# Kernel tuning notes

Measured on AMD Instinct MI355X. Metric: run time of the kernel, lower is better.

The kernel has to match this reference:

```python
import jax, jax.numpy as jnp
import numpy as np

B, NPG, H, HEADS, L, E, IN_DIM, FREQ = 4, 256, 128, 4, 6, 65536, 5, 256
N = B * NPG
C = H // HEADS  # per-head channels = 32


def _w(key, shape, fan_in):
    return jax.random.normal(key, shape, jnp.float32) * (fan_in ** -0.5)


def _ln(x):  # LayerNorm, elementwise_affine=False, eps=1e-5
    mu = jnp.mean(x, axis=-1, keepdims=True)
    var = jnp.mean((x - mu) ** 2, axis=-1, keepdims=True)
    return (x - mu) / jnp.sqrt(var + 1e-5)


def setup_inputs() -> dict:
    key = jax.random.key(0)
    ks = jax.random.split(key, 40)
    x = jax.random.normal(ks[0], (N, IN_DIM), jnp.float32)
    # edges constrained within each graph
    kg = jnp.repeat(jnp.arange(B), E // B)
    src = jax.random.randint(ks[1], (E,), 0, NPG) + kg * NPG
    dst = jax.random.randint(ks[2], (E,), 0, NPG) + kg * NPG
    edge_index = jnp.stack([src, dst]).astype(jnp.int32)
    batch = jnp.repeat(jnp.arange(B), NPG).astype(jnp.int32)
    time_matrix = jax.random.normal(ks[3], (N, N), jnp.float32)
    p = {}
    p['Wn'] = _w(ks[4], (IN_DIM, H), IN_DIM); p['bn'] = jnp.zeros((H,), jnp.float32)
    p['Wee'] = _w(ks[5], (1, 1), 1); p['bee'] = jnp.zeros((1,), jnp.float32)
    p['Wt1'] = _w(ks[6], (FREQ, H), FREQ); p['bt1'] = jnp.zeros((H,), jnp.float32)
    p['Wt2'] = _w(ks[7], (H, H), H); p['bt2'] = jnp.zeros((H,), jnp.float32)
    p['Wa'] = _w(ks[8], (L, H, 4 * H), H); p['ba'] = jnp.zeros((L, 4 * H), jnp.float32)
    p['Wq'] = _w(ks[9], (L, H, H), H); p['bq'] = jnp.zeros((L, H), jnp.float32)
    p['Wk'] = _w(ks[10], (L, H, H), H); p['bk'] = jnp.zeros((L, H), jnp.float32)
    p['Wv'] = _w(ks[11], (L, H, H), H); p['bv'] = jnp.zeros((L, H), jnp.float32)
    p['We'] = _w(ks[12], (L, 1, H), 1)  # lin_edge, bias=False in PyG
    p['Wskip'] = _w(ks[13], (L, H, H), H); p['bskip'] = jnp.zeros((L, H), jnp.float32)
    p['Wf1'] = _w(ks[14], (L, H, 2 * H), H); p['bf1'] = jnp.zeros((L, 2 * H), jnp.float32)
    p['Wf2'] = _w(ks[15], (L, 2 * H, H), 2 * H); p['bf2'] = jnp.zeros((L, H), jnp.float32)
    p['Wb'] = _w(ks[16], (H, H, H), H); p['bb'] = jnp.zeros((H,), jnp.float32)
    p['Wm1'] = _w(ks[17], (H, H), H); p['bm1'] = jnp.zeros((H,), jnp.float32)
    p['Wm2'] = _w(ks[18], (H, 4), H); p['bm2'] = jnp.zeros((4,), jnp.float32)
    return {'x': x, 'edge_index': edge_index, 'batch': batch, 't': 50,
            'time_matrix': time_matrix, **p}


def reference(x, edge_index, batch, t, time_matrix,
              Wn, bn, Wee, bee, Wt1, bt1, Wt2, bt2,
              Wa, ba, Wq, bq, Wk, bk, Wv, bv, We, Wskip, bskip,
              Wf1, bf1, Wf2, bf2, Wb, bb, Wm1, bm1, Wm2, bm2):
    h = x @ Wn + bn  # [N,H]
    # sinusoidal timestep embedding (dim=FREQ)
    half = FREQ // 2
    freqs = jnp.exp(-jnp.log(jnp.float32(10000.0)) * jnp.arange(half, dtype=jnp.float32) / half)
    targs = jnp.float32(t) * freqs
    emb = jnp.concatenate([jnp.cos(targs), jnp.sin(targs)])[None, :]  # [1,FREQ]
    t_emb = jax.nn.silu(emb @ Wt1 + bt1) @ Wt2 + bt2  # [1,H]
    t_mod = jax.nn.silu(t_emb)

    src, dst = edge_index[0], edge_index[1]
    edge_attr = time_matrix[src, dst][:, None] @ Wee + bee  # [E,1]

    inv_sqrt_c = jnp.float32(1.0 / np.sqrt(C))
    for l in range(L):
        ss = t_mod @ Wa[l] + ba[l]  # [1,4H]
        sh_msa, sc_msa, sh_mlp, sc_mlp = jnp.split(ss, 4, axis=1)
        hn = _ln(h) * (1 + sc_msa) + sh_msa
        # TransformerConv: gather per-edge Q/K/V, softmax over incoming edges of dst
        q = (hn @ Wq[l] + bq[l]).reshape(N, HEADS, C)
        k = (hn @ Wk[l] + bk[l]).reshape(N, HEADS, C)
        v = (hn @ Wv[l] + bv[l]).reshape(N, HEADS, C)
        e = (edge_attr @ We[l]).reshape(E, HEADS, C)
        kj = k[src] + e
        alpha = jnp.sum(q[dst] * kj, axis=-1) * inv_sqrt_c  # [E,HEADS]
        m = jax.ops.segment_max(alpha, dst, num_segments=N)
        a = jnp.exp(alpha - m[dst])
        s = jax.ops.segment_sum(a, dst, num_segments=N)
        a = a / (s[dst] + 1e-16)
        msg = (v[src] + e) * a[..., None]  # [E,HEADS,C]
        attn_out = jax.ops.segment_sum(msg, dst, num_segments=N).reshape(N, H)
        attn_out = attn_out + hn @ Wskip[l] + bskip[l]  # root/skip connection
        h = h + attn_out
        hn = _ln(h) * (1 + sc_mlp) + sh_mlp
        h = h + (jax.nn.gelu(hn @ Wf1[l] + bf1[l], approximate=False) @ Wf2[l] + bf2[l])

    # to_dense_batch: all graphs have NPG nodes -> reshape, full mask
    hd = h.reshape(B, NPG, H)
    # nn.Bilinear: pair[b,i,j,o] = h[b,i] @ Wb[o] @ h[b,j] + bb[o]
    tmp = jnp.einsum('bik,okl->biol', hd, Wb)  # [B,n,H,H]
    pair = jnp.einsum('biol,bjl->bijo', tmp, hd) + bb  # [B,n,n,H]
    logits = jax.nn.silu(pair @ Wm1 + bm1) @ Wm2 + bm2  # [B,n,n,4]
    return logits
```

## Files before the change

kernel.cpp:

```cpp
#include <hip/hip_runtime.h>
#include <math.h>

#define N_NODES 1024
#define HDIM 128
#define EDGES 65536
#define LAYERS 6

typedef __attribute__((ext_vector_type(8))) short bf16x8;
typedef __attribute__((ext_vector_type(4))) float f32x4;

#define OFF_H     0
#define OFF_Q     131072
#define OFF_K     262144
#define OFF_V     393216
#define OFF_SKP   524288
#define OFF_G     655360
#define OFF_SS    917504
#define OFF_EA    920576
#define OFF_CVEC  986112
#define OFF_INT   986240
#define OFF_M     1054912
#define OFF_U     3152064
#define OFF_MT    11540672
#define OFF_HB    12589248
#define OFF_WB    12654912

#define WM1T_OFF  786432

__device__ __forceinline__ float silu_f(float x) { return x / (1.f + expf(-x)); }
__device__ __forceinline__ float frcp(float x) { return __builtin_amdgcn_rcpf(x); }

__device__ __forceinline__ unsigned short f2bf(float f) {
    unsigned int u = __float_as_uint(f);
    u += 0x7FFFu + ((u >> 16) & 1u);
    return (unsigned short)(u >> 16);
}
__device__ __forceinline__ float bf2f(unsigned short s) {
    return __uint_as_float(((unsigned int)s) << 16);
}

__global__ __launch_bounds__(256) void k_ssf(const void* tptr,
    const float* __restrict__ Wt1, const float* __restrict__ bt1,
    const float* __restrict__ Wt2, const float* __restrict__ bt2,
    const float* __restrict__ bb, const float* __restrict__ Wm1, const float* __restrict__ bm1,
    const float* __restrict__ Wa, const float* __restrict__ ba,
    float* __restrict__ ss_all, float* __restrict__ cvec)
{
    __shared__ float emb_s[256];
    __shared__ float part[2][128];
    __shared__ float tmp1_s[128];
    __shared__ float tmod_s[128];
    int tid = threadIdx.x;
    int iv = *(const int*)tptr;
    float fv = __int_as_float(iv);
    float tval = (iv > -1000000 && iv < 1000000) ? (float)iv : fv;
    {
        int fi = tid & 127;
        float fr = expf(-logf(10000.f) * (float)fi / 128.f);
        float ta = tval * fr;
        emb_s[tid] = (tid < 128) ? cosf(ta) : sinf(ta);
    }
    __syncthreads();
    {
        int col = tid & 127, sl = tid >> 7;
        float p = 0.f;
#pragma unroll 8
        for (int i = sl * 128; i < sl * 128 + 128; i++) p += emb_s[i] * Wt1[i * 128 + col];
        part[sl][col] = p;
    }
    __syncthreads();
    if (tid < 128) tmp1_s[tid] = silu_f(bt1[tid] + part[0][tid] + part[1][tid]);
    __syncthreads();
    {
        int col = tid & 127, sl = tid >> 7;
        float p = 0.f;
#pragma unroll 8
        for (int i = sl * 64; i < sl * 64 + 64; i++) p += tmp1_s[i] * Wt2[i * 128 + col];
        part[sl][col] = p;
    }
    __syncthreads();
    if (tid < 128) tmod_s[tid] = silu_f(bt2[tid] + part[0][tid] + part[1][tid]);
    __syncthreads();
    {
        int idx = blockIdx.x * 256 + tid;
        int l = idx >> 9, j = idx & 511;
        float a = ba[l * 512 + j];
        const float* w = Wa + l * 65536 + j;
#pragma unroll 4
        for (int k = 0; k < 128; k++) a += tmod_s[k] * w[k * 512];
        ss_all[idx] = a;
    }
    if (blockIdx.x == 0) {
        {
            int col = tid & 127, sl = tid >> 7;
            float p = 0.f;
#pragma unroll 8
            for (int i = sl * 64; i < sl * 64 + 64; i++) p += bb[i] * Wm1[i * 128 + col];
            part[sl][col] = p;
        }
        __syncthreads();
        if (tid < 128) cvec[tid] = bm1[tid] + part[0][tid] + part[1][tid];
    }
}

__global__ __launch_bounds__(256) void k_wtrans(
    const float* __restrict__ Wq, const float* __restrict__ Wk,
    const float* __restrict__ Wv, const float* __restrict__ Wsk,
    const float* __restrict__ Wf1, const float* __restrict__ Wf2,
    const float* __restrict__ Wm1, short* __restrict__ WT)
{
    __shared__ __align__(16) short T[64][80];
    int t = blockIdx.x;
    int tid = threadIdx.x;
    const float* src; short* dst; int K, N, kt, nt;
    if (t < 96) {
        int mat = t >> 2, sub = t & 3;
        int l = mat >> 2, m = mat & 3;
        src = (m == 0 ? Wq : m == 1 ? Wk : m == 2 ? Wv : Wsk) + l * 16384;
        dst = WT + (size_t)mat * 16384;
        K = 128; N = 128; kt = sub >> 1; nt = sub & 1;
    } else if (t < 144) {
        int i = t - 96; int l = i >> 3, sub = i & 7;
        src = Wf1 + l * 32768;
        dst = WT + 24 * 16384 + (size_t)l * 32768;
        K = 128; N = 256; kt = sub & 1; nt = sub >> 1;
    } else if (t < 192) {
        int i = t - 144; int l = i >> 3, sub = i & 7;
        src = Wf2 + l * 32768;
        dst = WT + 24 * 16384 + 6 * 32768 + (size_t)l * 32768;
        K = 256; N = 128; kt = sub >> 1; nt = sub & 1;
    } else {
        int sub = t - 192;
        src = Wm1;
        dst = WT + WM1T_OFF;
        K = 128; N = 128; kt = sub >> 1; nt = sub & 1;
    }
    int k0 = kt * 64, n0 = nt * 64;
    for (int p = 0; p < 16; p++) {
        int idx = p * 256 + tid;
        int kk = idx >> 6, nn = idx & 63;
        T[nn][kk] = (short)f2bf(src[(k0 + kk) * N + n0 + nn]);
    }
    __syncthreads();
    for (int p = 0; p < 2; p++) {
        int idx = p * 256 + tid;
        int nn = idx >> 3, sq = idx & 7;
        *(int4*)&dst[(size_t)(n0 + nn) * K + k0 + sq * 8] = *(const int4*)&T[nn][sq * 8];
    }
}

__global__ __launch_bounds__(256) void k_inpedge(const float* __restrict__ x,
    const float* __restrict__ Wn, const float* __restrict__ bn, float* __restrict__ h,
    const int* __restrict__ ei, const float* __restrict__ tm,
    const float* __restrict__ Wee, const float* __restrict__ bee,
    float* __restrict__ ea, int* __restrict__ deg)
{
    int bid = blockIdx.x;
    int tid = threadIdx.x;
    if (bid < 512) {
        int idx = bid * 256 + tid;
        int i = idx >> 7, j = idx & 127;
        float acc = bn[j];
#pragma unroll
        for (int kk = 0; kk < 5; kk++) acc += x[i * 5 + kk] * Wn[kk * 128 + j];
        h[idx] = acc;
    } else {
        int e = (bid - 512) * 256 + tid;
        int s = ei[e], d = ei[EDGES + e];
        ea[e] = tm[s * N_NODES + d] * Wee[0] + bee[0];
        atomicAdd(&deg[d], 1);
    }
}

__global__ __launch_bounds__(1024) void k_scan(const int* __restrict__ deg, int* __restrict__ rowptr)
{
    __shared__ int tmp[1024];
    int tid = threadIdx.x;
    tmp[tid] = deg[tid];
    __syncthreads();
    for (int off = 1; off < 1024; off <<= 1) {
        int vv = (tid >= off) ? tmp[tid - off] : 0;
        __syncthreads();
        tmp[tid] += vv;
        __syncthreads();
    }
    rowptr[tid + 1] = tmp[tid];
    if (tid == 0) rowptr[0] = 0;
}

__global__ __launch_bounds__(256) void k_scatter(const int* __restrict__ ei,
    const int* __restrict__ rowptr, int* __restrict__ cursor, int* __restrict__ eorder)
{
    int e = blockIdx.x * 256 + threadIdx.x;
    int d = ei[EDGES + e];
    int pos = atomicAdd(&cursor[d], 1);
    eorder[rowptr[d] + pos] = e;
}

__global__ __launch_bounds__(128) void k_sort2(const int* __restrict__ rowptr,
    int* __restrict__ eorder, const int* __restrict__ ei, const float* __restrict__ ea,
    int* __restrict__ src_csr, float* __restrict__ ea_csr)
{
    __shared__ int key[256];
    int node = blockIdx.x;
    int tid = threadIdx.x;
    int beg = rowptr[node], end = rowptr[node + 1];
    int n = end - beg;
    if (n <= 256) {
        for (int i = tid; i < 256; i += 128) key[i] = (i < n) ? eorder[beg + i] : 0x7FFFFFFF;
        __syncthreads();
        for (int k = 2; k <= 256; k <<= 1) {
            for (int j = k >> 1; j > 0; j >>= 1) {
                int i = ((tid / j) * 2 * j) + (tid % j);
                int l = i + j;
                bool up = ((i & k) == 0);
                int a = key[i], b = key[l];
                if ((a > b) == up) { key[i] = b; key[l] = a; }
                __syncthreads();
            }
        }
        for (int i = tid; i < n; i += 128) {
            int e = key[i];
            src_csr[beg + i] = ei[e];
            ea_csr[beg + i] = ea[e];
        }
    } else {
        if (tid == 0) {
            for (int i = beg + 1; i < end; ++i) {
                int kk = eorder[i];
                int j = i - 1;
                while (j >= beg && eorder[j] > kk) { eorder[j + 1] = eorder[j]; --j; }
                eorder[j + 1] = kk;
            }
        }
        __syncthreads();
        for (int i = tid; i < n; i += 128) {
            int e = eorder[beg + i];
            src_csr[beg + i] = ei[e];
            ea_csr[beg + i] = ea[e];
        }
    }
}

__global__ __launch_bounds__(256) void k_qkvs(const float* __restrict__ h,
    const float* __restrict__ ss, const short* __restrict__ WT, int layer,
    const float* __restrict__ bq, const float* __restrict__ bk,
    const float* __restrict__ bv, const float* __restrict__ bsk,
    float* __restrict__ q, short* __restrict__ kb16, short* __restrict__ vb16,
    float* __restrict__ skp)
{
    __shared__ __align__(16) short As[16][136];
    __shared__ float shs[128], scs[128];
    int tid = threadIdx.x;
    int r0 = blockIdx.x * 16;
    if (tid < 128) { shs[tid] = ss[tid]; scs[tid] = ss[128 + tid]; }
    __syncthreads();
    {
        int row = tid >> 4, o = tid & 15;
        const float* hr = h + (size_t)(r0 + row) * 128 + o * 8;
        float s = 0.f, s2 = 0.f;
#pragma unroll
        for (int j = 0; j < 2; j++) {
            float4 vv = *(const float4*)&hr[j * 4];
            s += vv.x + vv.y + vv.z + vv.w;
            s2 += vv.x * vv.x + vv.y * vv.y + vv.z * vv.z + vv.w * vv.w;
        }
        s += __shfl_xor(s, 1, 64); s2 += __shfl_xor(s2, 1, 64);
        s += __shfl_xor(s, 2, 64); s2 += __shfl_xor(s2, 2, 64);
        s += __shfl_xor(s, 4, 64); s2 += __shfl_xor(s2, 4, 64);
        s += __shfl_xor(s, 8, 64); s2 += __shfl_xor(s2, 8, 64);
        float mu = s * (1.f / 128.f);
        float var = s2 * (1.f / 128.f) - mu * mu;
        float rs = rsqrtf(var + 1e-5f);
#pragma unroll
        for (int j = 0; j < 2; j++) {
            float4 vv = *(const float4*)&hr[j * 4];
            int cb = o * 8 + j * 4;
            short4 o4;
            o4.x = (short)f2bf((vv.x - mu) * rs * (1.f + scs[cb])     + shs[cb]);
            o4.y = (short)f2bf((vv.y - mu) * rs * (1.f + scs[cb + 1]) + shs[cb + 1]);
            o4.z = (short)f2bf((vv.z - mu) * rs * (1.f + scs[cb + 2]) + shs[cb + 2]);
            o4.w = (short)f2bf((vv.w - mu) * rs * (1.f + scs[cb + 3]) + shs[cb + 3]);
            *(short4*)&As[row][cb] = o4;
        }
    }
    __syncthreads();
    int w = tid >> 6, lane = tid & 63, c = lane & 15, g = lane >> 4;
    const short* Wm = WT + (size_t)(layer * 4 + w) * 16384;
    f32x4 acc[8] = {};
#pragma unroll
    for (int kq = 0; kq < 4; kq++) {
        int ko = kq * 32 + g * 8;
        bf16x8 a0 = *(const bf16x8*)&As[c][ko];
#pragma unroll
        for (int nt = 0; nt < 8; nt++) {
            bf16x8 bfr = *(const bf16x8*)&Wm[(size_t)(nt * 16 + c) * 128 + ko];
            acc[nt] = __builtin_amdgcn_mfma_f32_16x16x32_bf16(a0, bfr, acc[nt], 0, 0, 0);
        }
    }
    if (w == 0) {
#pragma unroll
        for (int nt = 0; nt < 8; nt++) {
            int n = nt * 16 + c;
            float bv2 = bq[n];
#pragma unroll
            for (int r = 0; r < 4; r++)
                q[(size_t)(r0 + g * 4 + r) * 128 + n] = acc[nt][r] + bv2;
        }
    } else if (w == 1) {
#pragma unroll
        for (int nt = 0; nt < 8; nt++) {
            int n = nt * 16 + c;
            float bv2 = bk[n];
#pragma unroll
            for (int r = 0; r < 4; r++)
                kb16[(size_t)(r0 + g * 4 + r) * 128 + n] = (short)f2bf(acc[nt][r] + bv2);
        }
    } else if (w == 2) {
#pragma unroll
        for (int nt = 0; nt < 8; nt++) {
            int n = nt * 16 + c;
            float bv2 = bv[n];
#pragma unroll
            for (int r = 0; r < 4; r++)
                vb16[(size_t)(r0 + g * 4 + r) * 128 + n] = (short)f2bf(acc[nt][r] + bv2);
        }
    } else {
#pragma unroll
        for (int nt = 0; nt < 8; nt++) {
            int n = nt * 16 + c;
            float bv2 = bsk[n];
#pragma unroll
            for (int r = 0; r < 4; r++)
                skp[(size_t)(r0 + g * 4 + r) * 128 + n] = acc[nt][r] + bv2;
        }
    }
}

__global__ __launch_bounds__(256) void k_ffn(float* __restrict__ h,
    const short* __restrict__ WT, int layer,
    const float* __restrict__ bf1, const float* __restrict__ bf2,
    const float* __restrict__ ss2, short* __restrict__ hb, int last)
{
    __shared__ __align__(16) short As[16][136];
    __shared__ __align__(16) short Gs[16][264];
    __shared__ float shs[128], scs[128];
    int tid = threadIdx.x;
    int r0 = blockIdx.x * 16;
    if (tid < 128) { shs[tid] = ss2[tid]; scs[tid] = ss2[128 + tid]; }
    __syncthreads();
    {
        int row = tid >> 4, o = tid & 15;
        const float* hr = h + (size_t)(r0 + row) * 128 + o * 8;
        float s = 0.f, s2 = 0.f;
#pragma unroll
        for (int j = 0; j < 2; j++) {
            float4 vv = *(const float4*)&hr[j * 4];
            s += vv.x + vv.y + vv.z + vv.w;
            s2 += vv.x * vv.x + vv.y * vv.y + vv.z * vv.z + vv.w * vv.w;
        }
        s += __shfl_xor(s, 1, 64); s2 += __shfl_xor(s2, 1, 64);
        s += __shfl_xor(s, 2, 64); s2 += __shfl_xor(s2, 2, 64);
        s += __shfl_xor(s, 4, 64); s2 += __shfl_xor(s2, 4, 64);
        s += __shfl_xor(s, 8, 64); s2 += __shfl_xor(s2, 8, 64);
        float mu = s * (1.f / 128.f);
        float var = s2 * (1.f / 128.f) - mu * mu;
        float rs = rsqrtf(var + 1e-5f);
#pragma unroll
        for (int j = 0; j < 2; j++) {
            float4 vv = *(const float4*)&hr[j * 4];
            int cb = o * 8 + j * 4;
            short4 o4;
            o4.x = (short)f2bf((vv.x - mu) * rs * (1.f + scs[cb])     + shs[cb]);
            o4.y = (short)f2bf((vv.y - mu) * rs * (1.f + scs[cb + 1]) + shs[cb + 1]);
            o4.z = (short)f2bf((vv.z - mu) * rs * (1.f + scs[cb + 2]) + shs[cb + 2]);
            o4.w = (short)f2bf((vv.w - mu) * rs * (1.f + scs[cb + 3]) + shs[cb + 3]);
            *(short4*)&As[row][cb] = o4;
        }
    }
    __syncthreads();
    int w = tid >> 6, lane = tid & 63, c = lane & 15, g = lane >> 4;
    const short* W1 = WT + 24 * 16384 + (size_t)layer * 32768;
    const short* W2 = WT + 24 * 16384 + 6 * 32768 + (size_t)layer * 32768;
    {
        f32x4 acc[4] = {};
#pragma unroll
        for (int kq = 0; kq < 4; kq++) {
            int ko = kq * 32 + g * 8;
            bf16x8 a0 = *(const bf16x8*)&As[c][ko];
#pragma unroll
            for (int nt = 0; nt < 4; nt++) {
                bf16x8 bfr = *(const bf16x8*)&W1[(size_t)(w * 64 + nt * 16 + c) * 128 + ko];
                acc[nt] = __builtin_amdgcn_mfma_f32_16x16x32_bf16(a0, bfr, acc[nt], 0, 0, 0);
            }
        }
#pragma unroll
        for (int nt = 0; nt < 4; nt++) {
            int n = w * 64 + nt * 16 + c;
            float bv = bf1[n];
#pragma unroll
            for (int r = 0; r < 4; r++) {
                float y = acc[nt][r] + bv;
                float gl = 0.5f * y * (1.f + erff(y * 0.70710678118654752f));
                Gs[g * 4 + r][n] = (short)f2bf(gl);
            }
        }
    }
    __syncthreads();
    {
        f32x4 acc2[2] = {};
#pragma unroll
        for (int kq = 0; kq < 8; kq++) {
            int ko = kq * 32 + g * 8;
            bf16x8 a0 = *(const bf16x8*)&Gs[c][ko];
#pragma unroll
            for (int nt2 = 0; nt2 < 2; nt2++) {
                bf16x8 bfr = *(const bf16x8*)&W2[(size_t)(w * 32 + nt2 * 16 + c) * 256 + ko];
                acc2[nt2] = __builtin_amdgcn_mfma_f32_16x16x32_bf16(a0, bfr, acc2[nt2], 0, 0, 0);
            }
        }
#pragma unroll
        for (int nt2 = 0; nt2 < 2; nt2++) {
            int n = w * 32 + nt2 * 16 + c;
            float bv = bf2[n];
#pragma unroll
            for (int r = 0; r < 4; r++) {
                int i = r0 + g * 4 + r;
                float nv = h[(size_t)i * 128 + n] + acc2[nt2][r] + bv;
                h[(size_t)i * 128 + n] = nv;
                if (last) hb[(size_t)i * 128 + n] = (short)f2bf(nv);
            }
        }
    }
}

__global__ __launch_bounds__(256) void k_attn(const float* __restrict__ q,
    const short* __restrict__ kb16, const short* __restrict__ vb16,
    const float* __restrict__ skp, float* __restrict__ h,
    const int* __restrict__ src_csr, const float* __restrict__ ea_csr,
    const float* __restrict__ We_l, const int* __restrict__ rowptr)
{
    __shared__ float ms[3][64], ssb[3][64], a0s[3][64], a1s[3][64];
    int tid = threadIdx.x;
    int wid = tid >> 6;
    int lane = tid & 63;
    int node = blockIdx.x;
    int c0 = lane * 2;
    float2 q2 = *(const float2*)&q[node * 128 + c0];
    float we0 = We_l[c0], we1 = We_l[c0 + 1];
    int beg = rowptr[node], end = rowptr[node + 1];
    int n = end - beg;
    int tb = beg + (n * wid) / 4;
    int te = beg + (n * (wid + 1)) / 4;
    float m = -INFINITY, s = 0.f, a0 = 0.f, a1 = 0.f;
    const float isc = 0.17677669529663687f;

    int t = tb;
    for (; t + 3 < te; t += 4) {
        int sn0 = src_csr[t],     sn1 = src_csr[t + 1];
        int sn2 = src_csr[t + 2], sn3 = src_csr[t + 3];
        float e0 = ea_csr[t],     e1 = ea_csr[t + 1];
        float e2 = ea_csr[t + 2], e3 = ea_csr[t + 3];
        ushort2 ku0 = *(const ushort2*)&kb16[sn0 * 128 + c0];
        ushort2 ku1 = *(const ushort2*)&kb16[sn1 * 128 + c0];
        ushort2 ku2 = *(const ushort2*)&kb16[sn2 * 128 + c0];
        ushort2 ku3 = *(const ushort2*)&kb16[sn3 * 128 + c0];
        ushort2 vu0 = *(const ushort2*)&vb16[sn0 * 128 + c0];
        ushort2 vu1 = *(const ushort2*)&vb16[sn1 * 128 + c0];
        ushort2 vu2 = *(const ushort2*)&vb16[sn2 * 128 + c0];
        ushort2 vu3 = *(const ushort2*)&vb16[sn3 * 128 + c0];
        float p0 = q2.x * (bf2f(ku0.x) + e0 * we0) + q2.y * (bf2f(ku0.y) + e0 * we1);
        float p1 = q2.x * (bf2f(ku1.x) + e1 * we0) + q2.y * (bf2f(ku1.y) + e1 * we1);
        float p2 = q2.x * (bf2f(ku2.x) + e2 * we0) + q2.y * (bf2f(ku2.y) + e2 * we1);
        float p3 = q2.x * (bf2f(ku3.x) + e3 * we0) + q2.y * (bf2f(ku3.y) + e3 * we1);
        p0 += __shfl_xor(p0, 1, 16); p1 += __shfl_xor(p1, 1, 16);
        p2 += __shfl_xor(p2, 1, 16); p3 += __shfl_xor(p3, 1, 16);
        p0 += __shfl_xor(p0, 2, 16); p1 += __shfl_xor(p1, 2, 16);
        p2 += __shfl_xor(p2, 2, 16); p3 += __shfl_xor(p3, 2, 16);
        p0 += __shfl_xor(p0, 4, 16); p1 += __shfl_xor(p1, 4, 16);
        p2 += __shfl_xor(p2, 4, 16); p3 += __shfl_xor(p3, 4, 16);
        p0 += __shfl_xor(p0, 8, 16); p1 += __shfl_xor(p1, 8, 16);
        p2 += __shfl_xor(p2, 8, 16); p3 += __shfl_xor(p3, 8, 16);
        {
            float al = p0 * isc;
            float mn = fmaxf(m, al);
            float scale = __expf(m - mn), wq = __expf(al - mn);
            s = s * scale + wq;
            a0 = a0 * scale + wq * (bf2f(vu0.x) + e0 * we0);
            a1 = a1 * scale + wq * (bf2f(vu0.y) + e0 * we1);
            m = mn;
        }
        {
            float al = p1 * isc;
            float mn = fmaxf(m, al);
            float scale = __expf(m - mn), wq = __expf(al - mn);
            s = s * scale + wq;
            a0 = a0 * scale + wq * (bf2f(vu1.x) + e1 * we0);
            a1 = a1 * scale + wq * (bf2f(vu1.y) + e1 * we1);
            m = mn;
        }
        {
            float al = p2 * isc;
            float mn = fmaxf(m, al);
            float scale = __expf(m - mn), wq = __expf(al - mn);
            s = s * scale + wq;
            a0 = a0 * scale + wq * (bf2f(vu2.x) + e2 * we0);
            a1 = a1 * scale + wq * (bf2f(vu2.y) + e2 * we1);
            m = mn;
        }
        {
            float al = p3 * isc;
            float mn = fmaxf(m, al);
            float scale = __expf(m - mn), wq = __expf(al - mn);
            s = s * scale + wq;
            a0 = a0 * scale + wq * (bf2f(vu3.x) + e3 * we0);
            a1 = a1 * scale + wq * (bf2f(vu3.y) + e3 * we1);
            m = mn;
        }
    }
    for (; t < te; ++t) {
        int sn = src_csr[t];
        float eav = ea_csr[t];
        ushort2 ku = *(const ushort2*)&kb16[sn * 128 + c0];
        ushort2 vu = *(const ushort2*)&vb16[sn * 128 + c0];
        float part = q2.x * (bf2f(ku.x) + eav * we0) + q2.y * (bf2f(ku.y) + eav * we1);
        part += __shfl_xor(part, 1, 16);
        part += __shfl_xor(part, 2, 16);
        part += __shfl_xor(part, 4, 16);
        part += __shfl_xor(part, 8, 16);
        float alpha = part * isc;
        float mn = fmaxf(m, alpha);
        float scale = __expf(m - mn), wq = __expf(alpha - mn);
        s = s * scale + wq;
        a0 = a0 * scale + wq * (bf2f(vu.x) + eav * we0);
        a1 = a1 * scale + wq * (bf2f(vu.y) + eav * we1);
        m = mn;
    }
    if (wid > 0) {
        ms[wid - 1][lane] = m; ssb[wid - 1][lane] = s;
        a0s[wid - 1][lane] = a0; a1s[wid - 1][lane] = a1;
    }
    __syncthreads();
    if (wid == 0) {
#pragma unroll
        for (int p = 0; p < 3; p++) {
            float mB = ms[p][lane], sB = ssb[p][lane];
            float b0 = a0s[p][lane], b1 = a1s[p][lane];
            float mm = fmaxf(m, mB);
            float eA = (m  > -1e30f) ? __expf(m  - mm) : 0.f;
            float eB = (mB > -1e30f) ? __expf(mB - mm) : 0.f;
            s = s * eA + sB * eB;
            a0 = a0 * eA + b0 * eB;
            a1 = a1 * eA + b1 * eB;
            m = mm;
        }
        float inv = (s > 0.f) ? 1.f / (s + 1e-16f) : 0.f;
        int o = node * 128 + c0;
        h[o]     += skp[o]     + a0 * inv;
        h[o + 1] += skp[o + 1] + a1 * inv;
    }
}

__global__ __launch_bounds__(256) void k_mprep(const float* __restrict__ Wb,
    const short* __restrict__ WT, float* __restrict__ M)
{
    __shared__ __align__(16) short Bls[128][136];
    int tid = threadIdx.x;
    int k = blockIdx.x;
    const short* Wm1T = WT + WM1T_OFF;
    {
        int lq = (tid & 31) * 4;
        int ob = tid >> 5;
        for (int it = 0; it < 16; it++) {
            int o = it * 8 + ob;
            float4 vv = *(const float4*)&Wb[(size_t)o * 16384 + k * 128 + lq];
            Bls[lq][o]     = (short)f2bf(vv.x);
            Bls[lq + 1][o] = (short)f2bf(vv.y);
            Bls[lq + 2][o] = (short)f2bf(vv.z);
            Bls[lq + 3][o] = (short)f2bf(vv.w);
        }
    }
    __syncthreads();
    int w = tid >> 6, lane = tid & 63, c = lane & 15, g = lane >> 4;
    f32x4 acc[2][8] = {};
#pragma unroll
    for (int kq = 0; kq < 4; kq++) {
        int ko = kq * 32 + g * 8;
        bf16x8 a0 = *(const bf16x8*)&Wm1T[(size_t)(w * 32 + c) * 128 + ko];
        bf16x8 a1 = *(const bf16x8*)&Wm1T[(size_t)(w * 32 + 16 + c) * 128 + ko];
#pragma unroll
        for (int nt = 0; nt < 8; nt++) {
            bf16x8 b = *(const bf16x8*)&Bls[nt * 16 + c][ko];
            acc[0][nt] = __builtin_amdgcn_mfma_f32_16x16x32_bf16(a0, b, acc[0][nt], 0, 0, 0);
            acc[1][nt] = __builtin_amdgcn_mfma_f32_16x16x32_bf16(a1, b, acc[1][nt], 0, 0, 0);
        }
    }
    float* Mk = M + (size_t)k * 16384;
#pragma unroll
    for (int it = 0; it < 2; it++)
#pragma unroll
        for (int nt = 0; nt < 8; nt++)
#pragma unroll
            for (int r = 0; r < 4; r++) {
                int m = w * 32 + it * 16 + g * 4 + r;
                int l = nt * 16 + c;
                Mk[m * 128 + l] = acc[it][nt][r];
            }
}

__global__ __launch_bounds__(256) void k_mtrans(const float* __restrict__ M,
                                                short* __restrict__ Mt)
{
    __shared__ __align__(16) short Ts[64][136];
    int tid = threadIdx.x;
    int n0 = blockIdx.x * 64;
    for (int p = 0; p < 32; p++) {
        int idx = p * 256 + tid;
        int k = idx >> 6, nn = idx & 63;
        Ts[nn][k] = (short)f2bf(M[(size_t)k * 16384 + n0 + nn]);
    }
    __syncthreads();
    for (int p = 0; p < 4; p++) {
        int idx = p * 256 + tid;
        int nn = idx >> 4, s = idx & 15;
        *(int4*)&Mt[(size_t)(n0 + nn) * 128 + s * 8] = *(const int4*)&Ts[nn][s * 8];
    }
}

__global__ __launch_bounds__(256) void k_p1(const short* __restrict__ hb,
    const short* __restrict__ Mt, short* __restrict__ U)
{
    __shared__ __align__(16) short As[128][72];
    __shared__ __align__(16) short Bs[128][72];
    int tid = threadIdx.x;
    int n0 = blockIdx.x * 128;
    int i0 = blockIdx.y * 128;
    int w = tid >> 6, lane = tid & 63, c = lane & 15, g = lane >> 4;
    f32x4 acc[2][8] = {};
    for (int kh = 0; kh < 2; kh++) {
        __syncthreads();
        for (int idx = tid; idx < 1024; idx += 256) {
            int r = idx >> 3, s = idx & 7;
            *(int4*)&As[r][s * 8] = *(const int4*)&hb[(i0 + r) * 128 + kh * 64 + s * 8];
            *(int4*)&Bs[r][s * 8] = *(const int4*)&Mt[(size_t)(n0 + r) * 128 + kh * 64 + s * 8];
        }
        __syncthreads();
#pragma unroll
        for (int kk = 0; kk < 2; kk++) {
            int ko = kk * 32 + g * 8;
            bf16x8 a0 = *(const bf16x8*)&As[w * 32 + c][ko];
            bf16x8 a1 = *(const bf16x8*)&As[w * 32 + 16 + c][ko];
#pragma unroll
            for (int nt = 0; nt < 8; nt++) {
                bf16x8 b = *(const bf16x8*)&Bs[nt * 16 + c][ko];
                acc[0][nt] = __builtin_amdgcn_mfma_f32_16x16x32_bf16(a0, b, acc[0][nt], 0, 0, 0);
                acc[1][nt] = __builtin_amdgcn_mfma_f32_16x16x32_bf16(a1, b, acc[1][nt], 0, 0, 0);
            }
        }
    }
#pragma unroll
    for (int it = 0; it < 2; it++)
#pragma unroll
        for (int nt = 0; nt < 8; nt++)
#pragma unroll
            for (int r = 0; r < 4; r++) {
                int i = i0 + w * 32 + it * 16 + g * 4 + r;
                int n = n0 + nt * 16 + c;
                U[(size_t)i * 16384 + n] = (short)f2bf(acc[it][nt][r]);
            }
}

__global__ __launch_bounds__(256) void k_p2(const short* __restrict__ hb,
    const short* __restrict__ U, const float* __restrict__ cvec,
    const float* __restrict__ Wm2, const float* __restrict__ bm2,
    float* __restrict__ out)
{
    __shared__ __align__(16) short Us[128][136];
    __shared__ float cvs[128];
    __shared__ float w2s[128][4];
    int tid = threadIdx.x;
    int i = blockIdx.x;
    int b = i >> 8;
    int w = tid >> 6, lane = tid & 63, c = lane & 15, g = lane >> 4;
    if (tid < 128) {
        cvs[tid] = cvec[tid];
        *(float4*)&w2s[tid][0] = *(const float4*)&Wm2[tid * 4];
    }
    for (int idx = tid; idx < 2048; idx += 256) {
        int r = idx >> 4, s = idx & 15;
        *(int4*)&Us[r][s * 8] = *(const int4*)&U[(size_t)i * 16384 + r * 128 + s * 8];
    }
    __syncthreads();
    float4 bmv = *(const float4*)&bm2[0];
#pragma unroll
    for (int jt = 0; jt < 4; jt++) {
        int jbase = w * 64 + jt * 16;
        bf16x8 hf[4];
        const short* hrow = hb + (size_t)(b * 256 + jbase + c) * 128;
#pragma unroll
        for (int kq = 0; kq < 4; kq++)
            hf[kq] = *(const bf16x8*)(hrow + kq * 32 + g * 8);
        f32x4 acc[8] = {};
#pragma unroll
        for (int kq = 0; kq < 4; kq++) {
            int ko = kq * 32 + g * 8;
#pragma unroll
            for (int mt = 0; mt < 8; mt++) {
                bf16x8 uv = *(const bf16x8*)&Us[mt * 16 + c][ko];
                acc[mt] = __builtin_amdgcn_mfma_f32_16x16x32_bf16(uv, hf[kq], acc[mt], 0, 0, 0);
            }
        }
        float p0 = 0.f, p1 = 0.f, p2 = 0.f, p3 = 0.f;
#pragma unroll
        for (int mt = 0; mt < 8; mt++) {
#pragma unroll
            for (int r = 0; r < 4; r++) {
                int m = mt * 16 + g * 4 + r;
                float y = acc[mt][r] + cvs[m];
                float sv = y * frcp(1.f + __expf(-y));
                p0 += sv * w2s[m][0]; p1 += sv * w2s[m][1];
                p2 += sv * w2s[m][2]; p3 += sv * w2s[m][3];
            }
        }
        p0 += __shfl_xor(p0, 16, 64); p1 += __shfl_xor(p1, 16, 64);
        p2 += __shfl_xor(p2, 16, 64); p3 += __shfl_xor(p3, 16, 64);
        p0 += __shfl_xor(p0, 32, 64); p1 += __shfl_xor(p1, 32, 64);
        p2 += __shfl_xor(p2, 32, 64); p3 += __shfl_xor(p3, 32, 64);
        if (g == 0) {
            int j = jbase + c;
            float4 o4 = { p0 + bmv.x, p1 + bmv.y, p2 + bmv.z, p3 + bmv.w };
            *(float4*)&out[((size_t)i * 256 + j) * 4] = o4;
        }
    }
}

extern "C" void kernel_launch(void* const* d_in, const int* in_sizes, int n_in,
                              void* d_out, int out_size, void* d_ws, size_t ws_size,
                              hipStream_t stream)
{
    const float* x   = (const float*)d_in[0];
    const int*   ei  = (const int*)d_in[1];
    const void*  tptr= d_in[3];
    const float* tm  = (const float*)d_in[4];
    const float* Wn  = (const float*)d_in[5];
    const float* bn  = (const float*)d_in[6];
    const float* Wee = (const float*)d_in[7];
    const float* bee = (const float*)d_in[8];
    const float* Wt1 = (const float*)d_in[9];
    const float* bt1 = (const float*)d_in[10];
    const float* Wt2 = (const float*)d_in[11];
    const float* bt2 = (const float*)d_in[12];
    const float* Wa  = (const float*)d_in[13];
    const float* ba  = (const float*)d_in[14];
    const float* Wq  = (const float*)d_in[15];
    const float* bq  = (const float*)d_in[16];
    const float* Wk  = (const float*)d_in[17];
    const float* bk  = (const float*)d_in[18];
    const float* Wv  = (const float*)d_in[19];
    const float* bv  = (const float*)d_in[20];
    const float* We  = (const float*)d_in[21];
    const float* Wsk = (const float*)d_in[22];
    const float* bsk = (const float*)d_in[23];
    const float* Wf1 = (const float*)d_in[24];
    const float* bf1 = (const float*)d_in[25];
    const float* Wf2 = (const float*)d_in[26];
    const float* bf2 = (const float*)d_in[27];
    const float* Wb  = (const float*)d_in[28];
    const float* bb  = (const float*)d_in[29];
    const float* Wm1 = (const float*)d_in[30];
    const float* bm1 = (const float*)d_in[31];
    const float* Wm2 = (const float*)d_in[32];
    const float* bm2 = (const float*)d_in[33];
    float* out = (float*)d_out;
    float* ws = (float*)d_ws;

    float* h    = ws + OFF_H;
    float* qb   = ws + OFF_Q;
    short* kb16 = (short*)(ws + OFF_K);
    short* vb16 = (short*)(ws + OFF_V);
    float* skp  = ws + OFF_SKP;
    float* ss   = ws + OFF_SS;
    float* ea   = ws + OFF_EA;
    float* cvec = ws + OFF_CVEC;
    int* iws    = (int*)(ws + OFF_INT);
    int* deg    = iws;
    int* cursor = iws + 1024;
    int* rowptr = iws + 2048;
    int* eorder = iws + 3073;
    int* src_csr   = (int*)(ws + OFF_G);
    float* ea_csr  = ws + OFF_G + 65536;
    float* Mst  = ws + OFF_M;
    short* Ub   = (short*)(ws + OFF_U);
    short* Mtb  = (short*)(ws + OFF_MT);
    short* hbb  = (short*)(ws + OFF_HB);
    short* WT   = (short*)(ws + OFF_WB);

    hipMemsetAsync(deg, 0, 2048 * sizeof(int), stream);
    k_ssf<<<12, 256, 0, stream>>>(tptr, Wt1, bt1, Wt2, bt2, bb, Wm1, bm1, Wa, ba, ss, cvec);
    k_wtrans<<<196, 256, 0, stream>>>(Wq, Wk, Wv, Wsk, Wf1, Wf2, Wm1, WT);
    k_inpedge<<<768, 256, 0, stream>>>(x, Wn, bn, h, ei, tm, Wee, bee, ea, deg);
    k_scan<<<1, 1024, 0, stream>>>(deg, rowptr);
    k_scatter<<<256, 256, 0, stream>>>(ei, rowptr, cursor, eorder);
    k_sort2<<<1024, 128, 0, stream>>>(rowptr, eorder, ei, ea, src_csr, ea_csr);

    for (int l = 0; l < LAYERS; l++) {
        const float* ssl = ss + l * 512;
        k_qkvs<<<64, 256, 0, stream>>>(h, ssl, WT, l,
            bq + l * 128, bk + l * 128, bv + l * 128, bsk + l * 128,
            qb, kb16, vb16, skp);
        k_attn<<<1024, 256, 0, stream>>>(qb, kb16, vb16, skp, h, src_csr, ea_csr,
                                         We + l * 128, rowptr);
        k_ffn<<<64, 256, 0, stream>>>(h, WT, l, bf1 + l * 256, bf2 + l * 128,
                                      ssl + 256, hbb, l == LAYERS - 1);
    }

    k_mprep<<<128, 256, 0, stream>>>(Wb, WT, Mst);
    k_mtrans<<<256, 256, 0, stream>>>(Mst, Mtb);
    k_p1<<<dim3(128, 8), 256, 0, stream>>>(hbb, Mtb, Ub);
    k_p2<<<1024, 256, 0, stream>>>(hbb, Ub, cvec, Wm2, bm2, out);
}
```

Measured before the change: 272.8 us.

## Split pair-logit kernel over j halves, preload h fragments, swizzle LDS U tile

Launches k_p2 with a second grid dimension so each block handles 128 of the 256 j columns, doubling the block count. Each wave now preloads its two h fragment sets before the main loop and reuses each LDS U read for two MFMAs. The padded LDS layout is replaced by an XOR-swizzled one to avoid bank conflicts. In exchange, every U row tile is loaded from global memory twice, once by each j-half block, and the wave holds more accumulator registers.

Measured after the change: 276.3 us. About the same (+1.3%).

```diff
diff --git a/kernel.cpp b/kernel.cpp
--- a/kernel.cpp
+++ b/kernel.cpp
@@ -675,48 +675,56 @@
     const float* __restrict__ Wm2, const float* __restrict__ bm2,
     float* __restrict__ out)
 {
-    __shared__ __align__(16) short Us[128][136];
+    __shared__ __align__(16) short Us[128][128];
     __shared__ float cvs[128];
     __shared__ float w2s[128][4];
     int tid = threadIdx.x;
     int i = blockIdx.x;
+    int jb = blockIdx.y;
     int b = i >> 8;
     int w = tid >> 6, lane = tid & 63, c = lane & 15, g = lane >> 4;
     if (tid < 128) {
         cvs[tid] = cvec[tid];
         *(float4*)&w2s[tid][0] = *(const float4*)&Wm2[tid * 4];
     }
+    bf16x8 hf[2][4];
+    {
+        const short* hrow = hb + (size_t)(b * 256 + jb * 128 + w * 32 + c) * 128;
+#pragma unroll
+        for (int jt = 0; jt < 2; jt++)
+#pragma unroll
+            for (int kq = 0; kq < 4; kq++)
+                hf[jt][kq] = *(const bf16x8*)(hrow + jt * 16 * 128 + kq * 32 + g * 8);
+    }
     for (int idx = tid; idx < 2048; idx += 256) {
         int r = idx >> 4, s = idx & 15;
-        *(int4*)&Us[r][s * 8] = *(const int4*)&U[(size_t)i * 16384 + r * 128 + s * 8];
-    }
-    __syncthreads();
+        int col = (s * 8) ^ ((r & 7) << 3);
+        *(int4*)&Us[r][col] = *(const int4*)&U[(size_t)i * 16384 + r * 128 + s * 8];
+    }
+    __syncthreads();
+    f32x4 acc[2][8] = {};
+#pragma unroll
+    for (int kq = 0; kq < 4; kq++) {
+        int ko = kq * 32 + g * 8;
+#pragma unroll
+        for (int mt = 0; mt < 8; mt++) {
+            int row = mt * 16 + c;
+            int col = ko ^ ((row & 7) << 3);
+            bf16x8 uv = *(const bf16x8*)&Us[row][col];
+            acc[0][mt] = __builtin_amdgcn_mfma_f32_16x16x32_bf16(uv, hf[0][kq], acc[0][mt], 0, 0, 0);
+            acc[1][mt] = __builtin_amdgcn_mfma_f32_16x16x32_bf16(uv, hf[1][kq], acc[1][mt], 0, 0, 0);
+        }
+    }
     float4 bmv = *(const float4*)&bm2[0];
 #pragma unroll
-    for (int jt = 0; jt < 4; jt++) {
-        int jbase = w * 64 + jt * 16;
-        bf16x8 hf[4];
-        const short* hrow = hb + (size_t)(b * 256 + jbase + c) * 128;
-#pragma unroll
-        for (int kq = 0; kq < 4; kq++)
-            hf[kq] = *(const bf16x8*)(hrow + kq * 32 + g * 8);
-        f32x4 acc[8] = {};
-#pragma unroll
-        for (int kq = 0; kq < 4; kq++) {
-            int ko = kq * 32 + g * 8;
-#pragma unroll
-            for (int mt = 0; mt < 8; mt++) {
-                bf16x8 uv = *(const bf16x8*)&Us[mt * 16 + c][ko];
-                acc[mt] = __builtin_amdgcn_mfma_f32_16x16x32_bf16(uv, hf[kq], acc[mt], 0, 0, 0);
-            }
-        }
+    for (int jt = 0; jt < 2; jt++) {
         float p0 = 0.f, p1 = 0.f, p2 = 0.f, p3 = 0.f;
 #pragma unroll
         for (int mt = 0; mt < 8; mt++) {
 #pragma unroll
             for (int r = 0; r < 4; r++) {
                 int m = mt * 16 + g * 4 + r;
-                float y = acc[mt][r] + cvs[m];
+                float y = acc[jt][mt][r] + cvs[m];
                 float sv = y * frcp(1.f + __expf(-y));
                 p0 += sv * w2s[m][0]; p1 += sv * w2s[m][1];
                 p2 += sv * w2s[m][2]; p3 += sv * w2s[m][3];
@@ -727,7 +735,7 @@
         p0 += __shfl_xor(p0, 32, 64); p1 += __shfl_xor(p1, 32, 64);
         p2 += __shfl_xor(p2, 32, 64); p3 += __shfl_xor(p3, 32, 64);
         if (g == 0) {
-            int j = jbase + c;
+            int j = jb * 128 + w * 32 + jt * 16 + c;
             float4 o4 = { p0 + bmv.x, p1 + bmv.y, p2 + bmv.z, p3 + bmv.w };
             *(float4*)&out[((size_t)i * 256 + j) * 4] = o4;
         }
@@ -817,5 +825,5 @@
     k_mprep<<<128, 256, 0, stream>>>(Wb, WT, Mst);
     k_mtrans<<<256, 256, 0, stream>>>(Mst, Mtb);
     k_p1<<<dim3(128, 8), 256, 0, stream>>>(hbb, Mtb, Ub);
-    k_p2<<<1024, 256, 0, stream>>>(hbb, Ub, cvec, Wm2, bm2, out);
-}
+    k_p2<<<dim3(1024, 2), 256, 0, stream>>>(hbb, Ub, cvec, Wm2, bm2, out);
+}
```
